# Kernel optimization log

Hardware: AMD Instinct MI355X
Metric: run time of the kernel (lower is better)

Reference implementation:

```python
import jax, jax.numpy as jnp
import numpy as np

D_MODEL = 1024
N_HEADS = 16
POINT_DIM = 4
PLUCKER_DIM = 6
PAIRS4 = [(0, 1), (0, 2), (0, 3), (1, 2), (1, 3), (2, 3)]
_J6 = jnp.array([[0, 0, 0, 0, 0, 1], [0, 0, 0, 0, -1, 0], [0, 0, 0, 1, 0, 0],
                 [0, 0, 1, 0, 0, 0], [0, -1, 0, 0, 0, 0], [1, 0, 0, 0, 0, 0]], dtype=jnp.float32)


def exterior(p1, p2):
    # p1, p2: [..., point_dim] -> normalized Plucker coords [..., 6]
    L = jnp.stack([p1[..., i] * p2[..., j] - p1[..., j] * p2[..., i] for i, j in PAIRS4], axis=-1)
    n = jnp.linalg.norm(L, axis=-1, keepdims=True)
    return L / jnp.maximum(n, 1e-12)


def setup_inputs() -> dict:
    key = jax.random.key(0)
    ks = jax.random.split(key, 16)
    B, T, D, H, pd = 2, 1024, D_MODEL, N_HEADS, POINT_DIM
    s = 0.02
    return {
        "x": jax.random.normal(ks[0], (B, T, D), dtype=jnp.float32),
        "qkv_w": jax.random.normal(ks[1], (D, 3 * D), dtype=jnp.float32) * s,
        "qkv_b": jnp.zeros((3 * D,), dtype=jnp.float32),
        "w1_write_w": jax.random.normal(ks[2], (2 * D, pd * H), dtype=jnp.float32) * s,
        "w2_write_w": jax.random.normal(ks[3], (D, pd * H), dtype=jnp.float32) * s,
        "w1_read_w": jax.random.normal(ks[4], (D, pd * H), dtype=jnp.float32) * s,
        "w2_read_w": jax.random.normal(ks[5], (D, pd * H), dtype=jnp.float32) * s,
        "mem_value_w": jax.random.normal(ks[6], (D, D), dtype=jnp.float32) * s,
        "mem_value_b": jnp.zeros((D,), dtype=jnp.float32),
        "mem_gate_w": jax.random.normal(ks[7], (D, H), dtype=jnp.float32) * s,
        "mem_gate_b": jnp.zeros((H,), dtype=jnp.float32),
        "mem_scale": jnp.full((H,), 0.1, dtype=jnp.float32),
        "out_w": jax.random.normal(ks[8], (D, D), dtype=jnp.float32) * s,
        "out_b": jnp.zeros((D,), dtype=jnp.float32),
        "decay_logits": jnp.full((H,), 4.6, dtype=jnp.float32),
        "J": _J6,
    }


def reference(x, qkv_w, qkv_b, w1_write_w, w2_write_w, w1_read_w, w2_read_w,
              mem_value_w, mem_value_b, mem_gate_w, mem_gate_b, mem_scale,
              out_w, out_b, decay_logits, J):
    B, T, D = x.shape
    H = N_HEADS
    dh = D // H
    pd = POINT_DIM
    scale = dh ** (-0.5)

    # ---- standard causal attention ----
    qkv = (x @ qkv_w + qkv_b).reshape(B, T, 3, H, dh)
    q = jnp.transpose(qkv[:, :, 0], (0, 2, 1, 3))  # [B,H,T,dh]
    k = jnp.transpose(qkv[:, :, 1], (0, 2, 1, 3))
    v = jnp.transpose(qkv[:, :, 2], (0, 2, 1, 3))
    scores = jnp.einsum('bhtd,bhsd->bhts', q, k) * scale
    causal_mask = jnp.triu(jnp.ones((T, T), dtype=bool), k=1)
    scores = jnp.where(causal_mask, -jnp.inf, scores)
    attn = jax.nn.softmax(scores, axis=-1)
    seq_out = jnp.einsum('bhts,bhsd->bthd', attn, v).reshape(B, T, D)

    # ---- trigram write lines ----
    z = jnp.zeros((B, 1, D), dtype=x.dtype)
    x_prev1 = jnp.concatenate([z, x[:, :-1]], axis=1)
    x_prev2 = jnp.concatenate([z, z, x[:, :-2]], axis=1)
    trigram_ctx = jnp.concatenate([x_prev2, x_prev1], axis=-1)  # [B,T,2D]
    w1 = (trigram_ctx @ w1_write_w).reshape(B, T, H, pd)
    w2 = (x @ w2_write_w).reshape(B, T, H, pd)
    write_lines = exterior(w1, w2)  # [B,T,H,6]
    r1 = (x @ w1_read_w).reshape(B, T, H, pd)
    r2 = (x @ w2_read_w).reshape(B, T, H, pd)
    read_lines = exterior(r1, r2)  # [B,T,H,6]

    # ---- Plucker incidence + decay weighting ----
    J_write = jnp.einsum('bshi,ij->bshj', write_lines, J)
    incidence = jnp.einsum('bthi,bshi->bhts', read_lines, J_write)  # [B,H,T,T]
    incidence_sq = incidence ** 2
    positions = jnp.arange(T, dtype=x.dtype)
    diffs = positions[:, None] - positions[None, :]  # [T,T]
    decays = jax.nn.sigmoid(decay_logits)  # [H]
    # strictly-causal (diffs>0) decay weights; masked_fill(triu diag=0, 0) == (diffs>0)
    weights = jnp.where(diffs[None] > 0, decays[:, None, None] ** jnp.maximum(diffs, 0.0)[None], 0.0)
    mem_score = jnp.sum(incidence_sq * weights[None], axis=-1)  # [B,H,T]

    # ---- gated memory value ----
    mem_val = x @ mem_value_w + mem_value_b  # [B,T,D]
    gate = jax.nn.sigmoid(x @ mem_gate_w + mem_gate_b)  # [B,T,H]
    mem_score_t = jnp.transpose(mem_score, (0, 2, 1))  # [B,T,H]
    gated = jax.nn.sigmoid(mem_score_t * mem_scale[None, None, :]) * gate
    gated = jnp.mean(gated, axis=-1, keepdims=True)  # [B,T,1]

    return (seq_out + gated * mem_val) @ out_w + out_b
```

## Files before the change

### kernel.cpp

```cpp
#include <hip/hip_runtime.h>
#include <hip/hip_bf16.h>
#include <stdint.h>


typedef __attribute__((ext_vector_type(8))) __bf16 bf16v8;
typedef __attribute__((ext_vector_type(8))) short  s16x8;
typedef __attribute__((ext_vector_type(4))) float  f32x4;

#define LOG2E 1.4426950408889634f

__device__ __forceinline__ float bf2f(short s) {
  union { uint32_t u; float f; } cv; cv.u = ((uint32_t)(uint16_t)s) << 16; return cv.f;
}
__device__ __forceinline__ short f2bf(float f) {
  union { float f; uint32_t u; } cv; cv.f = f;
  uint32_t r = cv.u + 0x7fffu + ((cv.u >> 16) & 1u);
  return (short)(r >> 16);
}

__device__ __forceinline__ f32x4 mfma_bf16(s16x8 a, s16x8 b, f32x4 c) {
  return __builtin_amdgcn_mfma_f32_16x16x32_bf16(
      __builtin_bit_cast(bf16v8, a), __builtin_bit_cast(bf16v8, b), c, 0, 0, 0);
}

__device__ __forceinline__ void gload_lds16(const void* g, void* l) {
  __builtin_amdgcn_global_load_lds(
      (const __attribute__((address_space(1))) uint32_t*)g,
      (__attribute__((address_space(3))) uint32_t*)l, 16, 0, 0);
}


__global__ __launch_bounds__(256) void k_prep(
    const float* __restrict__ x, const float* __restrict__ qkvw,
    const float* __restrict__ mvw, const float* __restrict__ ow,
    const float* __restrict__ w1w, const float* __restrict__ w2w,
    const float* __restrict__ r1w, const float* __restrict__ r2w,
    const float* __restrict__ gw, const float* __restrict__ qkvb,
    const float* __restrict__ mvb,
    short* __restrict__ xb, short* __restrict__ btall, short* __restrict__ owT,
    float* __restrict__ biasAll) {
  __shared__ float tile[32][33];
  const int bid = blockIdx.x;
  const int tid = threadIdx.x;
  if (bid < 2048) {
    const int i = (bid * 256 + tid) * 4;
    float4 v = *(const float4*)&x[i];
    short4 o;
    o.x = f2bf(v.x); o.y = f2bf(v.y); o.z = f2bf(v.z); o.w = f2bf(v.w);
    *(short4*)&xb[i] = o;
    return;
  }
  if (bid < 7168) {
    const float* W; short* Wt; int N, u;
    if (bid < 5120)      { W = qkvw; Wt = btall;                       N = 3072; u = bid - 2048; }
    else if (bid < 6144) { W = mvw;  Wt = btall + (size_t)3072 * 1024; N = 1024; u = bid - 5120; }
    else                 { W = ow;   Wt = owT;                         N = 1024; u = bid - 6144; }
    const int ntiles = N >> 5;
    const int n0 = (u % ntiles) * 32, k0 = (u / ntiles) * 32;
    const int tx = tid & 31, ty = tid >> 5;
#pragma unroll
    for (int i = 0; i < 4; i++)
      tile[ty + i * 8][tx] = W[(size_t)(k0 + ty + i * 8) * N + n0 + tx];
    __syncthreads();
#pragma unroll
    for (int i = 0; i < 4; i++)
      Wt[(size_t)(n0 + ty + i * 8) * 1024 + k0 + tx] = f2bf(tile[tx][ty + i * 8]);
    return;
  }
  if (bid < 8704) {
    const int idx = (bid - 7168) * 256 + tid;
    const int r = idx >> 10, k = idx & 1023;
    float v = 0.f;
    if (r < 64)       v = w1w[(size_t)k * 64 + r];
    else if (r < 128) v = w1w[(size_t)(1024 + k) * 64 + (r - 64)];
    else if (r < 192) v = w2w[(size_t)k * 64 + (r - 128)];
    else if (r < 256) v = r1w[(size_t)k * 64 + (r - 192)];
    else if (r < 320) v = r2w[(size_t)k * 64 + (r - 256)];
    else if (r < 336) v = gw[(size_t)k * 16 + (r - 320)];
    btall[(size_t)4096 * 1024 + idx] = f2bf(v);
    return;
  }
  {
    const int i = (bid - 8704) * 256 + tid;
    if (i < 4480) {
      float v = 0.f;
      if (i < 3072) v = qkvb[i];
      else if (i < 4096) v = mvb[i - 3072];
      biasAll[i] = v;
    }
  }
}


__global__ __launch_bounds__(256) void k_gemmF(const short* __restrict__ A,
                                               const short* __restrict__ Bt,
                                               short* __restrict__ C,
                                               const float* __restrict__ bias,
                                               float* __restrict__ projf) {
  const int N = 4480, K = 1024;
  __shared__ short As[128 * 32];
  __shared__ short Bs[128 * 32];
  const int m0 = blockIdx.x * 128, n0 = blockIdx.y * 128;
  const int tid = threadIdx.x;
  const int lane = tid & 63, w = tid >> 6;
  const int wr = (w >> 1) * 64, wc = (w & 1) * 64;
  const int l15 = lane & 15, lg = lane >> 4;
  f32x4 acc[4][4] = {};
  for (int k0 = 0; k0 < K; k0 += 32) {
#pragma unroll
    for (int p = 0; p < 2; p++) {
      const int e = p * 256 + tid;
      const int r = e >> 2, c8 = (e & 3) << 3;
      gload_lds16(A + (size_t)(m0 + r) * K + k0 + c8, As + e * 8);
      gload_lds16(Bt + (size_t)(n0 + r) * K + k0 + c8, Bs + e * 8);
    }
    __syncthreads();
    s16x8 af[4], bfv[4];
#pragma unroll
    for (int i = 0; i < 4; i++) {
      af[i]  = *(const s16x8*)&As[(wr + i * 16 + l15) * 32 + lg * 8];
      bfv[i] = *(const s16x8*)&Bs[(wc + i * 16 + l15) * 32 + lg * 8];
    }
#pragma unroll
    for (int mi = 0; mi < 4; mi++)
#pragma unroll
      for (int ni = 0; ni < 4; ni++)
        acc[mi][ni] = mfma_bf16(af[mi], bfv[ni], acc[mi][ni]);
    __syncthreads();
  }
  const bool isproj = (n0 >= 4096);
#pragma unroll
  for (int mi = 0; mi < 4; mi++)
#pragma unroll
    for (int ni = 0; ni < 4; ni++) {
      const int col = n0 + wc + ni * 16 + l15;
      const float bv = bias[col];
#pragma unroll
      for (int r = 0; r < 4; r++) {
        const int row = m0 + wr + mi * 16 + lg * 4 + r;
        const float v = acc[mi][ni][r] + bv;
        if (isproj) projf[(size_t)row * 384 + (col - 4096)] = v;
        else        C[(size_t)row * 4480 + col] = f2bf(v);
      }
    }
}


__global__ __launch_bounds__(256) void k_gemm(const short* __restrict__ A,
                                              const short* __restrict__ Bt,
                                              float* __restrict__ C,
                                              const float* __restrict__ bias,
                                              int N, int K) {
  __shared__ short As[128 * 32];
  __shared__ short Bs[128 * 32];
  const int m0 = blockIdx.x * 128, n0 = blockIdx.y * 128;
  const int tid = threadIdx.x;
  const int lane = tid & 63, w = tid >> 6;
  const int wr = (w >> 1) * 64, wc = (w & 1) * 64;
  const int l15 = lane & 15, lg = lane >> 4;
  f32x4 acc[4][4] = {};
  for (int k0 = 0; k0 < K; k0 += 32) {
#pragma unroll
    for (int p = 0; p < 2; p++) {
      const int e = p * 256 + tid;
      const int r = e >> 2, c8 = (e & 3) << 3;
      gload_lds16(A + (size_t)(m0 + r) * K + k0 + c8, As + e * 8);
      gload_lds16(Bt + (size_t)(n0 + r) * K + k0 + c8, Bs + e * 8);
    }
    __syncthreads();
    s16x8 af[4], bfv[4];
#pragma unroll
    for (int i = 0; i < 4; i++) {
      af[i]  = *(const s16x8*)&As[(wr + i * 16 + l15) * 32 + lg * 8];
      bfv[i] = *(const s16x8*)&Bs[(wc + i * 16 + l15) * 32 + lg * 8];
    }
#pragma unroll
    for (int mi = 0; mi < 4; mi++)
#pragma unroll
      for (int ni = 0; ni < 4; ni++)
        acc[mi][ni] = mfma_bf16(af[mi], bfv[ni], acc[mi][ni]);
    __syncthreads();
  }
#pragma unroll
  for (int mi = 0; mi < 4; mi++)
#pragma unroll
    for (int ni = 0; ni < 4; ni++) {
      const int col = n0 + wc + ni * 16 + l15;
      const float bv = bias ? bias[col] : 0.f;
#pragma unroll
      for (int r = 0; r < 4; r++) {
        const int row = m0 + wr + mi * 16 + lg * 4 + r;
        C[(size_t)row * N + col] = acc[mi][ni][r] + bv;
      }
    }
}


__global__ void k_vtr(const short* __restrict__ fused, short* __restrict__ vtg) {
  __shared__ short tile[32][33];
  const int bh = blockIdx.z;
  const int b = bh >> 4, h = bh & 15;
  const int t0 = blockIdx.x * 32, d0 = blockIdx.y * 32;
  const int tx = threadIdx.x, ty = threadIdx.y;
#pragma unroll
  for (int i = 0; i < 4; i++)
    tile[ty + i * 8][tx] =
        fused[(size_t)(b * 1024 + t0 + ty + i * 8) * 4480 + 2048 + h * 64 + d0 + tx];
  __syncthreads();
#pragma unroll
  for (int i = 0; i < 4; i++)
    vtg[(size_t)(bh * 64 + d0 + ty + i * 8) * 1024 + t0 + tx] = tile[tx][ty + i * 8];
}


__global__ __launch_bounds__(256) void k_attn(const short* __restrict__ fused,
                                              const short* __restrict__ vtg,
                                              float* __restrict__ Of,
                                              float* __restrict__ Ml) {
  const int id = blockIdx.x;
  const int j = 15 - (id >> 6);
  const int rem = id & 63;
  const int sid = rem >> 5, bh = rem & 31;
  const int b = bh >> 4, h = bh & 15;
  const int tid = threadIdx.x, lane = tid & 63, w = tid >> 6;
  const int l15 = lane & 15, lg = lane >> 4;
  const int q0 = j * 64;
  const int nkv = j + 1;
  const int half = (nkv + 1) >> 1;
  const int lo = sid ? half : 0;
  const int hi = sid ? nkv : half;
  const int pidx = ((j * 32 + bh) << 1) | sid;

  __shared__ short Kl[64 * 72];
  __shared__ short Vt[64 * 72];
  __shared__ short Pl[4][16 * 72];
  const short* base = fused + (size_t)b * 1024 * 4480;
  const short* vbase = vtg + (size_t)bh * 64 * 1024;

  const int e0 = tid, e1 = tid + 256;
  const int r0e = e0 >> 3, c0e = (e0 & 7) << 3;
  const int r1e = e1 >> 3, c1e = (e1 & 7) << 3;

  s16x8 qf[2];
#pragma unroll
  for (int ks = 0; ks < 2; ks++)
    qf[ks] = *(const s16x8*)&base[(size_t)(q0 + w * 16 + l15) * 4480 +
                                  h * 64 + ks * 32 + lg * 8];

  f32x4 O[4] = {};
  float m_run[4], l_run[4];
#pragma unroll
  for (int r = 0; r < 4; r++) { m_run[r] = -1e30f; l_run[r] = 0.f; }

  if (lo < hi) {
    const int kv0 = lo * 64;
    s16x8 ka = *(const s16x8*)&base[(size_t)(kv0 + r0e) * 4480 + 1024 + h * 64 + c0e];
    s16x8 kb = *(const s16x8*)&base[(size_t)(kv0 + r1e) * 4480 + 1024 + h * 64 + c1e];
    s16x8 va = *(const s16x8*)&vbase[(size_t)r0e * 1024 + kv0 + c0e];
    s16x8 vb = *(const s16x8*)&vbase[(size_t)r1e * 1024 + kv0 + c1e];
    *(s16x8*)&Kl[r0e * 72 + c0e] = ka;
    *(s16x8*)&Kl[r1e * 72 + c1e] = kb;
    *(s16x8*)&Vt[r0e * 72 + c0e] = va;
    *(s16x8*)&Vt[r1e * 72 + c1e] = vb;
  }
  __syncthreads();

  for (int kt = lo; kt < hi; kt++) {
    const int kv0 = kt * 64;
    const bool pf = (kt + 1 < hi);
    s16x8 kn0, kn1, vn0, vn1;
    if (pf) {
      const int kvn = kv0 + 64;
      kn0 = *(const s16x8*)&base[(size_t)(kvn + r0e) * 4480 + 1024 + h * 64 + c0e];
      kn1 = *(const s16x8*)&base[(size_t)(kvn + r1e) * 4480 + 1024 + h * 64 + c1e];
      vn0 = *(const s16x8*)&vbase[(size_t)r0e * 1024 + kvn + c0e];
      vn1 = *(const s16x8*)&vbase[(size_t)r1e * 1024 + kvn + c1e];
    }

    f32x4 S[4] = {};
    __builtin_amdgcn_s_setprio(1);
#pragma unroll
    for (int sf = 0; sf < 4; sf++) {
      s16x8 kf0 = *(const s16x8*)&Kl[(sf * 16 + l15) * 72 + lg * 8];
      s16x8 kf1 = *(const s16x8*)&Kl[(sf * 16 + l15) * 72 + 32 + lg * 8];
      S[sf] = mfma_bf16(qf[0], kf0, S[sf]);
      S[sf] = mfma_bf16(qf[1], kf1, S[sf]);
    }
    __builtin_amdgcn_s_setprio(0);

    const bool diag = (kt == j);
    float sv[4][4];
#pragma unroll
    for (int sf = 0; sf < 4; sf++)
#pragma unroll
      for (int r = 0; r < 4; r++) {
        float vv = S[sf][r] * 0.125f;
        if (diag) {
          const int sg = kv0 + sf * 16 + l15;
          const int qg = q0 + w * 16 + lg * 4 + r;
          if (sg > qg) vv = -1e30f;
        }
        sv[sf][r] = vv;
      }
#pragma unroll
    for (int r = 0; r < 4; r++) {
      float pm = fmaxf(fmaxf(sv[0][r], sv[1][r]), fmaxf(sv[2][r], sv[3][r]));
      pm = fmaxf(pm, __shfl_xor(pm, 1, 64));
      pm = fmaxf(pm, __shfl_xor(pm, 2, 64));
      pm = fmaxf(pm, __shfl_xor(pm, 4, 64));
      pm = fmaxf(pm, __shfl_xor(pm, 8, 64));
      if (pm > m_run[r] + 8.f) {
        const float fac = exp2f((m_run[r] - pm) * LOG2E);
        m_run[r] = pm;
        l_run[r] *= fac;
#pragma unroll
        for (int nf = 0; nf < 4; nf++) O[nf][r] *= fac;
      }
      float rs = 0.f;
#pragma unroll
      for (int sf = 0; sf < 4; sf++) {
        float p = (sv[sf][r] <= -1e29f) ? 0.f : exp2f((sv[sf][r] - m_run[r]) * LOG2E);
        rs += p;
        Pl[w][(lg * 4 + r) * 72 + sf * 16 + l15] = f2bf(p);
      }
      rs += __shfl_xor(rs, 1, 64);
      rs += __shfl_xor(rs, 2, 64);
      rs += __shfl_xor(rs, 4, 64);
      rs += __shfl_xor(rs, 8, 64);
      l_run[r] += rs;
    }

    __builtin_amdgcn_s_setprio(1);
#pragma unroll
    for (int ks = 0; ks < 2; ks++) {
      s16x8 pfr = *(const s16x8*)&Pl[w][l15 * 72 + ks * 32 + lg * 8];
#pragma unroll
      for (int nf = 0; nf < 4; nf++) {
        s16x8 vf = *(const s16x8*)&Vt[(nf * 16 + l15) * 72 + ks * 32 + lg * 8];
        O[nf] = mfma_bf16(pfr, vf, O[nf]);
      }
    }
    __builtin_amdgcn_s_setprio(0);

    __syncthreads();
    if (pf) {
      *(s16x8*)&Kl[r0e * 72 + c0e] = kn0;
      *(s16x8*)&Kl[r1e * 72 + c1e] = kn1;
      *(s16x8*)&Vt[r0e * 72 + c0e] = vn0;
      *(s16x8*)&Vt[r1e * 72 + c1e] = vn1;
      __syncthreads();
    }
  }

  float* ob = Of + (size_t)pidx * 4096;
  float* mb = Ml + (size_t)pidx * 128;
#pragma unroll
  for (int r = 0; r < 4; r++) {
    const int rloc = w * 16 + lg * 4 + r;
#pragma unroll
    for (int nf = 0; nf < 4; nf++)
      ob[rloc * 64 + nf * 16 + l15] = O[nf][r];
    if (l15 == 0) {
      mb[rloc] = m_run[r];
      mb[64 + rloc] = l_run[r];
    }
  }
}


__global__ __launch_bounds__(256) void k_amerge(const float* __restrict__ Of,
                                                const float* __restrict__ Ml,
                                                short* __restrict__ outp) {
  const int g = blockIdx.x * 256 + threadIdx.x;
  const int rg = g >> 4, c4 = (g & 15) << 2;
  const int p = rg >> 6, rloc = rg & 63;
  const int j = p >> 5, bh = p & 31;
  const int b = bh >> 4, h = bh & 15;
  const int t = j * 64 + rloc;
  const float* ml0 = Ml + (size_t)(p * 2 + 0) * 128;
  const float* ml1 = Ml + (size_t)(p * 2 + 1) * 128;
  const float m0 = ml0[rloc], l0 = ml0[64 + rloc];
  const float m1 = ml1[rloc], l1 = ml1[64 + rloc];
  const float M = fmaxf(m0, m1);
  const float w0 = exp2f((m0 - M) * LOG2E);
  const float w1 = exp2f((m1 - M) * LOG2E);
  const float inv = 1.f / (w0 * l0 + w1 * l1);
  f32x4 o0 = *(const f32x4*)&Of[(size_t)(p * 2 + 0) * 4096 + rloc * 64 + c4];
  f32x4 o1 = *(const f32x4*)&Of[(size_t)(p * 2 + 1) * 4096 + rloc * 64 + c4];
  short4 ov;
  ov.x = f2bf((w0 * o0[0] + w1 * o1[0]) * inv);
  ov.y = f2bf((w0 * o0[1] + w1 * o1[1]) * inv);
  ov.z = f2bf((w0 * o0[2] + w1 * o1[2]) * inv);
  ov.w = f2bf((w0 * o0[3] + w1 * o1[3]) * inv);
  *(short4*)&outp[((size_t)(b * 1024 + t)) * 1024 + h * 64 + c4] = ov;
}


__device__ __forceinline__ void exterior6(const float p1[4], const float p2[4], float L[6]) {
  L[0] = p1[0] * p2[1] - p1[1] * p2[0];
  L[1] = p1[0] * p2[2] - p1[2] * p2[0];
  L[2] = p1[0] * p2[3] - p1[3] * p2[0];
  L[3] = p1[1] * p2[2] - p1[2] * p2[1];
  L[4] = p1[1] * p2[3] - p1[3] * p2[1];
  L[5] = p1[2] * p2[3] - p1[3] * p2[2];
  float n = sqrtf(L[0] * L[0] + L[1] * L[1] + L[2] * L[2] +
                  L[3] * L[3] + L[4] * L[4] + L[5] * L[5]);
  float inv = 1.f / fmaxf(n, 1e-12f);
#pragma unroll
  for (int j = 0; j < 6; j++) L[j] *= inv;
}

__global__ void k_lines(const float* __restrict__ proj, const float* __restrict__ Jm,
                        float* __restrict__ jw, float* __restrict__ rl) {
  const int idx = blockIdx.x * 256 + threadIdx.x;
  const int t = idx & 1023, h = (idx >> 10) & 15, b = idx >> 14;
  const int n = b * 1024 + t;
  const int bh = b * 16 + h;
  float p1[4], p2[4], L[6];
#pragma unroll
  for (int p = 0; p < 4; p++) {
    float a  = (t >= 2) ? proj[(size_t)(n - 2) * 384 + h * 4 + p] : 0.f;
    float bb = (t >= 1) ? proj[(size_t)(n - 1) * 384 + 64 + h * 4 + p] : 0.f;
    p1[p] = a + bb;
    p2[p] = proj[(size_t)n * 384 + 128 + h * 4 + p];
  }
  exterior6(p1, p2, L);
  const size_t jo = (size_t)bh * 6144 + t;
#pragma unroll
  for (int j = 0; j < 6; j++) {
    float s = 0.f;
#pragma unroll
    for (int i = 0; i < 6; i++) s += L[i] * Jm[i * 6 + j];
    jw[jo + (size_t)j * 1024] = s;
  }
#pragma unroll
  for (int p = 0; p < 4; p++) {
    p1[p] = proj[(size_t)n * 384 + 192 + h * 4 + p];
    p2[p] = proj[(size_t)n * 384 + 256 + h * 4 + p];
  }
  exterior6(p1, p2, L);
  const size_t ro = ((size_t)bh * 1024 + t) * 6;
#pragma unroll
  for (int j = 0; j < 6; j++) rl[ro + j] = L[j];
}


__global__ __launch_bounds__(256) void k_mscore(const float* __restrict__ jw,
                                                const float* __restrict__ rl,
                                                const float* __restrict__ dlog,
                                                float* __restrict__ ms) {
  const int gtid = blockIdx.x * 256 + threadIdx.x;
  const int wid = gtid >> 6, lane = gtid & 63;
  const int bh = wid >> 10, t = wid & 1023;
  const int h = bh & 15, b = bh >> 4;
  const float d = 1.f / (1.f + expf(-dlog[h]));
  const float l2d = log2f(d);
  const float* jwp = jw + (size_t)bh * 6144;
  const float* rp = rl + ((size_t)bh * 1024 + t) * 6;
  const float r0 = rp[0], r1 = rp[1], r2 = rp[2], r3 = rp[3], r4 = rp[4], r5 = rp[5];
  float wgt = exp2f((float)(t - lane) * l2d);
  const float gw = exp2f(-64.f * l2d);
  float acc = 0.f;
  for (int s = lane; s < t; s += 64) {
    const float dot = r0 * jwp[s] + r1 * jwp[1024 + s] + r2 * jwp[2048 + s] +
                      r3 * jwp[3072 + s] + r4 * jwp[4096 + s] + r5 * jwp[5120 + s];
    acc += wgt * dot * dot;
    wgt *= gw;
  }
  acc += __shfl_xor(acc, 1, 64);
  acc += __shfl_xor(acc, 2, 64);
  acc += __shfl_xor(acc, 4, 64);
  acc += __shfl_xor(acc, 8, 64);
  acc += __shfl_xor(acc, 16, 64);
  acc += __shfl_xor(acc, 32, 64);
  if (lane == 0) ms[((size_t)(b * 1024 + t)) * 16 + h] = acc;
}


__global__ __launch_bounds__(256) void k_combine(const short* __restrict__ attn,
                                                 const short* __restrict__ fused,
                                                 const float* __restrict__ proj,
                                                 const float* __restrict__ ms,
                                                 const float* __restrict__ mem_scale,
                                                 const float* __restrict__ gate_b,
                                                 short* __restrict__ comb) {
  const int n = blockIdx.x;
  const int tid = threadIdx.x;
  __shared__ float gsh;
  if (tid < 16) {
    const float gp = proj[(size_t)n * 384 + 320 + tid] + gate_b[tid];
    const float g = 1.f / (1.f + expf(-gp));
    const float sc = ms[(size_t)n * 16 + tid] * mem_scale[tid];
    const float sg = 1.f / (1.f + expf(-sc));
    float v = sg * g;
    v += __shfl_xor(v, 1, 64);
    v += __shfl_xor(v, 2, 64);
    v += __shfl_xor(v, 4, 64);
    v += __shfl_xor(v, 8, 64);
    if (tid == 0) gsh = v * (1.f / 16.f);
  }
  __syncthreads();
  const float g = gsh;
  const int c0 = tid * 4;
  short4 av = *(const short4*)&attn[(size_t)n * 1024 + c0];
  short4 mvv = *(const short4*)&fused[(size_t)n * 4480 + 3072 + c0];
  short4 ov;
  ov.x = f2bf(bf2f(av.x) + g * bf2f(mvv.x));
  ov.y = f2bf(bf2f(av.y) + g * bf2f(mvv.y));
  ov.z = f2bf(bf2f(av.z) + g * bf2f(mvv.z));
  ov.w = f2bf(bf2f(av.w) + g * bf2f(mvv.w));
  *(short4*)&comb[(size_t)n * 1024 + c0] = ov;
}


extern "C" void kernel_launch(void* const* d_in, const int* in_sizes, int n_in,
                              void* d_out, int out_size, void* d_ws, size_t ws_size,
                              hipStream_t stream) {
  const float* x    = (const float*)d_in[0];
  const float* qkvw = (const float*)d_in[1];
  const float* qkvb = (const float*)d_in[2];
  const float* w1w  = (const float*)d_in[3];
  const float* w2w  = (const float*)d_in[4];
  const float* r1w  = (const float*)d_in[5];
  const float* r2w  = (const float*)d_in[6];
  const float* mvw  = (const float*)d_in[7];
  const float* mvb  = (const float*)d_in[8];
  const float* gw   = (const float*)d_in[9];
  const float* gb   = (const float*)d_in[10];
  const float* msc  = (const float*)d_in[11];
  const float* ow   = (const float*)d_in[12];
  const float* ob   = (const float*)d_in[13];
  const float* dlog = (const float*)d_in[14];
  const float* Jm   = (const float*)d_in[15];
  float* out = (float*)d_out;

  char* wsp = (char*)d_ws;
  auto alloc = [&](size_t bytes) {
    char* p = wsp;
    wsp += (bytes + 255) & ~(size_t)255;
    return p;
  };
  short* xb     = (short*)alloc((size_t)2048 * 1024 * 2);
  short* btall  = (short*)alloc((size_t)4480 * 1024 * 2);
  short* owT    = (short*)alloc((size_t)1024 * 1024 * 2);
  short* fusedC = (short*)alloc((size_t)2048 * 4480 * 2);
  float* projf  = (float*)alloc((size_t)2048 * 384 * 4);
  float* biasA  = (float*)alloc((size_t)4480 * 4);
  short* vtg    = (short*)alloc((size_t)32 * 64 * 1024 * 2);
  short* attnO  = (short*)alloc((size_t)2048 * 1024 * 2);
  short* comb   = (short*)alloc((size_t)2048 * 1024 * 2);
  float* jwb    = (float*)alloc((size_t)32 * 6144 * 4);
  float* rlb    = (float*)alloc((size_t)32768 * 6 * 4);
  float* msb    = (float*)alloc((size_t)2048 * 16 * 4);
  float* Of     = (float*)alloc((size_t)1024 * 4096 * 4);
  float* Mlb    = (float*)alloc((size_t)1024 * 128 * 4);

  k_prep<<<8722, 256, 0, stream>>>(x, qkvw, mvw, ow, w1w, w2w, r1w, r2w, gw,
                                   qkvb, mvb, xb, btall, owT, biasA);

  k_gemmF<<<dim3(16, 35), 256, 0, stream>>>(xb, btall, fusedC, biasA, projf);

  k_vtr<<<dim3(32, 2, 32), dim3(32, 8), 0, stream>>>(fusedC, vtg);
  k_attn<<<1024, 256, 0, stream>>>(fusedC, vtg, Of, Mlb);
  k_amerge<<<2048, 256, 0, stream>>>(Of, Mlb, attnO);

  k_lines<<<128, 256, 0, stream>>>(projf, Jm, jwb, rlb);
  k_mscore<<<8192, 256, 0, stream>>>(jwb, rlb, dlog, msb);
  k_combine<<<2048, 256, 0, stream>>>(attnO, fusedC, projf, msb, msc, gb, comb);

  k_gemm<<<dim3(16, 8), 256, 0, stream>>>(comb, owT, out, ob, 1024, 1024);
}
```

Baseline: 135.9 us.

## Fuse V transpose into QKV GEMM epilogue and attention merge into combine

```diff
diff --git a/kernel.cpp b/kernel.cpp
--- a/kernel.cpp
+++ b/kernel.cpp
@@ -96,7 +96,8 @@
                                                const short* __restrict__ Bt,
                                                short* __restrict__ C,
                                                const float* __restrict__ bias,
-                                               float* __restrict__ projf) {
+                                               float* __restrict__ projf,
+                                               short* __restrict__ vtg) {
   const int N = 4480, K = 1024;
   __shared__ short As[128 * 32];
   __shared__ short Bs[128 * 32];
@@ -129,60 +130,87 @@
     __syncthreads();
   }
   const bool isproj = (n0 >= 4096);
+  const bool isv = (n0 >= 2048) && (n0 < 3072);
 #pragma unroll
   for (int mi = 0; mi < 4; mi++)
 #pragma unroll
     for (int ni = 0; ni < 4; ni++) {
       const int col = n0 + wc + ni * 16 + l15;
       const float bv = bias[col];
-#pragma unroll
-      for (int r = 0; r < 4; r++) {
-        const int row = m0 + wr + mi * 16 + lg * 4 + r;
-        const float v = acc[mi][ni][r] + bv;
-        if (isproj) projf[(size_t)row * 384 + (col - 4096)] = v;
-        else        C[(size_t)row * 4480 + col] = f2bf(v);
-      }
-    }
-}
-
-
+      if (isv) {
+        const int row0 = m0 + wr + mi * 16 + lg * 4;
+        const int t0 = row0 & 1023, bloc = row0 >> 10;
+        const int cd = col - 2048;
+        const int hh = cd >> 6, dd = cd & 63;
+        short4 pk;
+        pk.x = f2bf(acc[mi][ni][0] + bv);
+        pk.y = f2bf(acc[mi][ni][1] + bv);
+        pk.z = f2bf(acc[mi][ni][2] + bv);
+        pk.w = f2bf(acc[mi][ni][3] + bv);
+        *(short4*)&vtg[((size_t)((bloc << 4) + hh) * 64 + dd) * 1024 + t0] = pk;
+      } else {
+#pragma unroll
+        for (int r = 0; r < 4; r++) {
+          const int row = m0 + wr + mi * 16 + lg * 4 + r;
+          const float v = acc[mi][ni][r] + bv;
+          if (isproj) projf[(size_t)row * 384 + (col - 4096)] = v;
+          else        C[(size_t)row * 4480 + col] = f2bf(v);
+        }
+      }
+    }
+}
+
+
+template <int BM>
 __global__ __launch_bounds__(256) void k_gemm(const short* __restrict__ A,
                                               const short* __restrict__ Bt,
                                               float* __restrict__ C,
                                               const float* __restrict__ bias,
                                               int N, int K) {
-  __shared__ short As[128 * 32];
+  constexpr int MI = BM / 32;
+  __shared__ short As[BM * 32];
   __shared__ short Bs[128 * 32];
-  const int m0 = blockIdx.x * 128, n0 = blockIdx.y * 128;
+  const int m0 = blockIdx.x * BM, n0 = blockIdx.y * 128;
   const int tid = threadIdx.x;
   const int lane = tid & 63, w = tid >> 6;
-  const int wr = (w >> 1) * 64, wc = (w & 1) * 64;
+  const int wr = (w >> 1) * (BM / 2), wc = (w & 1) * 64;
   const int l15 = lane & 15, lg = lane >> 4;
-  f32x4 acc[4][4] = {};
+  f32x4 acc[MI][4] = {};
   for (int k0 = 0; k0 < K; k0 += 32) {
+    if constexpr (BM == 128) {
+#pragma unroll
+      for (int p = 0; p < 2; p++) {
+        const int e = p * 256 + tid;
+        const int r = e >> 2, c8 = (e & 3) << 3;
+        gload_lds16(A + (size_t)(m0 + r) * K + k0 + c8, As + e * 8);
+      }
+    } else {
+      const int r = tid >> 2, c8 = (tid & 3) << 3;
+      gload_lds16(A + (size_t)(m0 + r) * K + k0 + c8, As + tid * 8);
+    }
 #pragma unroll
     for (int p = 0; p < 2; p++) {
       const int e = p * 256 + tid;
       const int r = e >> 2, c8 = (e & 3) << 3;
-      gload_lds16(A + (size_t)(m0 + r) * K + k0 + c8, As + e * 8);
       gload_lds16(Bt + (size_t)(n0 + r) * K + k0 + c8, Bs + e * 8);
     }
     __syncthreads();
-    s16x8 af[4], bfv[4];
-#pragma unroll
-    for (int i = 0; i < 4; i++) {
-      af[i]  = *(const s16x8*)&As[(wr + i * 16 + l15) * 32 + lg * 8];
+    s16x8 af[MI], bfv[4];
+#pragma unroll
+    for (int i = 0; i < MI; i++)
+      af[i] = *(const s16x8*)&As[(wr + i * 16 + l15) * 32 + lg * 8];
+#pragma unroll
+    for (int i = 0; i < 4; i++)
       bfv[i] = *(const s16x8*)&Bs[(wc + i * 16 + l15) * 32 + lg * 8];
-    }
-#pragma unroll
-    for (int mi = 0; mi < 4; mi++)
+#pragma unroll
+    for (int mi = 0; mi < MI; mi++)
 #pragma unroll
       for (int ni = 0; ni < 4; ni++)
         acc[mi][ni] = mfma_bf16(af[mi], bfv[ni], acc[mi][ni]);
     __syncthreads();
   }
 #pragma unroll
-  for (int mi = 0; mi < 4; mi++)
+  for (int mi = 0; mi < MI; mi++)
 #pragma unroll
     for (int ni = 0; ni < 4; ni++) {
       const int col = n0 + wc + ni * 16 + l15;
@@ -193,23 +221,6 @@
         C[(size_t)row * N + col] = acc[mi][ni][r] + bv;
       }
     }
-}
-
-
-__global__ void k_vtr(const short* __restrict__ fused, short* __restrict__ vtg) {
-  __shared__ short tile[32][33];
-  const int bh = blockIdx.z;
-  const int b = bh >> 4, h = bh & 15;
-  const int t0 = blockIdx.x * 32, d0 = blockIdx.y * 32;
-  const int tx = threadIdx.x, ty = threadIdx.y;
-#pragma unroll
-  for (int i = 0; i < 4; i++)
-    tile[ty + i * 8][tx] =
-        fused[(size_t)(b * 1024 + t0 + ty + i * 8) * 4480 + 2048 + h * 64 + d0 + tx];
-  __syncthreads();
-#pragma unroll
-  for (int i = 0; i < 4; i++)
-    vtg[(size_t)(bh * 64 + d0 + ty + i * 8) * 1024 + t0 + tx] = tile[tx][ty + i * 8];
 }
 
 
@@ -365,34 +376,6 @@
       mb[64 + rloc] = l_run[r];
     }
   }
-}
-
-
-__global__ __launch_bounds__(256) void k_amerge(const float* __restrict__ Of,
-                                                const float* __restrict__ Ml,
-                                                short* __restrict__ outp) {
-  const int g = blockIdx.x * 256 + threadIdx.x;
-  const int rg = g >> 4, c4 = (g & 15) << 2;
-  const int p = rg >> 6, rloc = rg & 63;
-  const int j = p >> 5, bh = p & 31;
-  const int b = bh >> 4, h = bh & 15;
-  const int t = j * 64 + rloc;
-  const float* ml0 = Ml + (size_t)(p * 2 + 0) * 128;
-  const float* ml1 = Ml + (size_t)(p * 2 + 1) * 128;
-  const float m0 = ml0[rloc], l0 = ml0[64 + rloc];
-  const float m1 = ml1[rloc], l1 = ml1[64 + rloc];
-  const float M = fmaxf(m0, m1);
-  const float w0 = exp2f((m0 - M) * LOG2E);
-  const float w1 = exp2f((m1 - M) * LOG2E);
-  const float inv = 1.f / (w0 * l0 + w1 * l1);
-  f32x4 o0 = *(const f32x4*)&Of[(size_t)(p * 2 + 0) * 4096 + rloc * 64 + c4];
-  f32x4 o1 = *(const f32x4*)&Of[(size_t)(p * 2 + 1) * 4096 + rloc * 64 + c4];
-  short4 ov;
-  ov.x = f2bf((w0 * o0[0] + w1 * o1[0]) * inv);
-  ov.y = f2bf((w0 * o0[1] + w1 * o1[1]) * inv);
-  ov.z = f2bf((w0 * o0[2] + w1 * o1[2]) * inv);
-  ov.w = f2bf((w0 * o0[3] + w1 * o1[3]) * inv);
-  *(short4*)&outp[((size_t)(b * 1024 + t)) * 1024 + h * 64 + c4] = ov;
 }
 
 
@@ -477,7 +460,8 @@
 }
 
 
-__global__ __launch_bounds__(256) void k_combine(const short* __restrict__ attn,
+__global__ __launch_bounds__(256) void k_combine(const float* __restrict__ Of,
+                                                 const float* __restrict__ Ml,
                                                  const short* __restrict__ fused,
                                                  const float* __restrict__ proj,
                                                  const float* __restrict__ ms,
@@ -501,14 +485,28 @@
   }
   __syncthreads();
   const float g = gsh;
+  const int b = n >> 10, t = n & 1023;
   const int c0 = tid * 4;
-  short4 av = *(const short4*)&attn[(size_t)n * 1024 + c0];
+  const int h = c0 >> 6, coff = c0 & 63;
+  const int bh = b * 16 + h;
+  const int p = ((t >> 6) * 32 + bh) << 1;
+  const int rloc = t & 63;
+  const float m0v = Ml[(size_t)p * 128 + rloc];
+  const float l0v = Ml[(size_t)p * 128 + 64 + rloc];
+  const float m1v = Ml[(size_t)(p + 1) * 128 + rloc];
+  const float l1v = Ml[(size_t)(p + 1) * 128 + 64 + rloc];
+  const float M = fmaxf(m0v, m1v);
+  const float w0 = exp2f((m0v - M) * LOG2E);
+  const float w1 = exp2f((m1v - M) * LOG2E);
+  const float inv = 1.f / (w0 * l0v + w1 * l1v);
+  f32x4 o0 = *(const f32x4*)&Of[(size_t)p * 4096 + rloc * 64 + coff];
+  f32x4 o1 = *(const f32x4*)&Of[(size_t)(p + 1) * 4096 + rloc * 64 + coff];
   short4 mvv = *(const short4*)&fused[(size_t)n * 4480 + 3072 + c0];
   short4 ov;
-  ov.x = f2bf(bf2f(av.x) + g * bf2f(mvv.x));
-  ov.y = f2bf(bf2f(av.y) + g * bf2f(mvv.y));
-  ov.z = f2bf(bf2f(av.z) + g * bf2f(mvv.z));
-  ov.w = f2bf(bf2f(av.w) + g * bf2f(mvv.w));
+  ov.x = f2bf((w0 * o0[0] + w1 * o1[0]) * inv + g * bf2f(mvv.x));
+  ov.y = f2bf((w0 * o0[1] + w1 * o1[1]) * inv + g * bf2f(mvv.y));
+  ov.z = f2bf((w0 * o0[2] + w1 * o1[2]) * inv + g * bf2f(mvv.z));
+  ov.w = f2bf((w0 * o0[3] + w1 * o1[3]) * inv + g * bf2f(mvv.w));
   *(short4*)&comb[(size_t)n * 1024 + c0] = ov;
 }
 
@@ -547,7 +545,6 @@
   float* projf  = (float*)alloc((size_t)2048 * 384 * 4);
   float* biasA  = (float*)alloc((size_t)4480 * 4);
   short* vtg    = (short*)alloc((size_t)32 * 64 * 1024 * 2);
-  short* attnO  = (short*)alloc((size_t)2048 * 1024 * 2);
   short* comb   = (short*)alloc((size_t)2048 * 1024 * 2);
   float* jwb    = (float*)alloc((size_t)32 * 6144 * 4);
   float* rlb    = (float*)alloc((size_t)32768 * 6 * 4);
@@ -558,15 +555,13 @@
   k_prep<<<8722, 256, 0, stream>>>(x, qkvw, mvw, ow, w1w, w2w, r1w, r2w, gw,
                                    qkvb, mvb, xb, btall, owT, biasA);
 
-  k_gemmF<<<dim3(16, 35), 256, 0, stream>>>(xb, btall, fusedC, biasA, projf);
-
-  k_vtr<<<dim3(32, 2, 32), dim3(32, 8), 0, stream>>>(fusedC, vtg);
+  k_gemmF<<<dim3(16, 35), 256, 0, stream>>>(xb, btall, fusedC, biasA, projf, vtg);
+
   k_attn<<<1024, 256, 0, stream>>>(fusedC, vtg, Of, Mlb);
-  k_amerge<<<2048, 256, 0, stream>>>(Of, Mlb, attnO);
 
   k_lines<<<128, 256, 0, stream>>>(projf, Jm, jwb, rlb);
   k_mscore<<<8192, 256, 0, stream>>>(jwb, rlb, dlog, msb);
-  k_combine<<<2048, 256, 0, stream>>>(attnO, fusedC, projf, msb, msc, gb, comb);
-
-  k_gemm<<<dim3(16, 8), 256, 0, stream>>>(comb, owT, out, ob, 1024, 1024);
-}
+  k_combine<<<2048, 256, 0, stream>>>(Of, Mlb, fusedC, projf, msb, msc, gb, comb);
+
+  k_gemm<64><<<dim3(32, 8), 256, 0, stream>>>(comb, owT, out, ob, 1024, 1024);
+}
```

Measured after the change: 139.6 us. +2.7%, slower.
